# Performance work log

Hardware: AMD Instinct MI355X
Metric: run time of the kernel (lower is better)

Reference implementation:

```python
import jax, jax.numpy as jnp
import numpy as np


def setup_inputs() -> dict:
    key = jax.random.key(0)
    k0, k1, k2, k3 = jax.random.split(key, 4)
    B, T, D, F, E = 4, 2048, 512, 1024, 8
    x = jax.random.normal(k0, (B, T, D), dtype=jnp.float32)
    # router weight is zero-init in the original; use small random values so top-k
    router_w = 0.02 * jax.random.normal(k1, (E, D), dtype=jnp.float32)
    router_b = jnp.zeros((E,), dtype=jnp.float32)
    w_gate_up = 0.02 * jax.random.normal(k2, (E, D, 2 * F), dtype=jnp.float32)
    w_down = 0.02 * jax.random.normal(k3, (E, F, D), dtype=jnp.float32)
    return {"x": x, "router_w": router_w, "router_b": router_b,
            "w_gate_up": w_gate_up, "w_down": w_down, "top_k": 2}


def reference(x, router_w, router_b, w_gate_up, w_down, top_k):
    B, T, D = x.shape
    E = router_w.shape[0]
    x_flat = x.reshape(-1, D)                      # [N, D]
    N = x_flat.shape[0]

    # router: softmax over experts, top-k, renormalize
    logits = x_flat @ router_w.T + router_b       # [N, E]
    probs = jax.nn.softmax(logits, axis=-1)
    top_w, top_idx = jax.lax.top_k(probs, top_k)  # [N, k]
    top_w = top_w / jnp.sum(top_w, axis=-1, keepdims=True)

    # scatter renormalized weights into a dense [N, E] combine matrix
    combine = jnp.zeros((N, E), dtype=x.dtype).at[
        jnp.arange(N)[:, None], top_idx].add(top_w)

    # per-expert SwiGLU; combine weights zero out non-selected experts, giving
    # math identical to the sort/gather/scatter dispatch in the original
    out = jnp.zeros_like(x_flat)
    for e in range(E):  # fixed small expert count, not a data-dim loop
        gate_up = x_flat @ w_gate_up[e]           # [N, 2F]
        gate, up = jnp.split(gate_up, 2, axis=-1)
        h = jax.nn.silu(gate) * up                # [N, F]
        out = out + combine[:, e:e + 1] * (h @ w_down[e])
    return out.reshape(B, T, D)
```

## Files before the change

kernel.cpp:

```cpp
#include <hip/hip_runtime.h>
#include <stdint.h>

#define N_TOK 8192
#define D_DIM 512
#define F_DIM 1024
#define E_NUM 8
#define M_SLOTS (N_TOK * 2)

typedef __bf16 bf16x8 __attribute__((ext_vector_type(8)));
typedef float f32x4 __attribute__((ext_vector_type(4)));

__device__ __forceinline__ ushort f2b(float f) {
    union { float f; unsigned u; } v; v.f = f;
    unsigned r = v.u + 0x7fffu + ((v.u >> 16) & 1u);
    return (ushort)(r >> 16);
}
__device__ __forceinline__ float b2f(ushort u) {
    union { unsigned i; float f; } v; v.i = ((unsigned)u) << 16; return v.f;
}
__device__ __forceinline__ void gload16(const void* g, void* l) {
    __builtin_amdgcn_global_load_lds(
        (const __attribute__((address_space(1))) unsigned int*)g,
        (__attribute__((address_space(3))) unsigned int*)l, 16, 0, 0);
}

__global__ __launch_bounds__(256) void transpose_k(const float* __restrict__ in,
                                                   ushort* __restrict__ out,
                                                   int R, int C) {
    __shared__ ushort tile[64][65];
    int e = blockIdx.z;
    const float* src = in + (size_t)e * R * C;
    ushort* dst = out + (size_t)e * R * C;
    int c0 = blockIdx.x * 64, r0 = blockIdx.y * 64;
#pragma unroll
    for (int i = 0; i < 4; ++i) {
        int ch = threadIdx.x + i * 256;
        int row = ch >> 4, pos = ch & 15;
        float4 v = *(const float4*)(src + (size_t)(r0 + row) * C + c0 + pos * 4);
        tile[row][pos * 4 + 0] = f2b(v.x);
        tile[row][pos * 4 + 1] = f2b(v.y);
        tile[row][pos * 4 + 2] = f2b(v.z);
        tile[row][pos * 4 + 3] = f2b(v.w);
    }
    __syncthreads();
#pragma unroll
    for (int i = 0; i < 2; ++i) {
        int ch = threadIdx.x + i * 256;
        int ocol = ch >> 3, rb = ch & 7;
        ushort tmp[8];
#pragma unroll
        for (int j = 0; j < 8; ++j) tmp[j] = tile[rb * 8 + j][ocol];
        *(uint4*)(dst + (size_t)(c0 + ocol) * R + r0 + rb * 8) = *(const uint4*)tmp;
    }
}

__global__ __launch_bounds__(256) void logits_k(const float* __restrict__ x,
                                                const float* __restrict__ rw,
                                                const float* __restrict__ rb,
                                                ushort* __restrict__ x_bf,
                                                int* __restrict__ tok_e,
                                                float* __restrict__ tok_w,
                                                int* __restrict__ cnt) {
    if (blockIdx.x == 0 && threadIdx.x < 16) cnt[threadIdx.x] = 0;
    int lane = threadIdx.x & 63, wv = threadIdx.x >> 6;
    int t = blockIdx.x * 4 + wv;
    float4 xa = *(const float4*)(x + (size_t)t * D_DIM + lane * 8);
    float4 xb = *(const float4*)(x + (size_t)t * D_DIM + lane * 8 + 4);
    ushort u[8] = {f2b(xa.x), f2b(xa.y), f2b(xa.z), f2b(xa.w),
                   f2b(xb.x), f2b(xb.y), f2b(xb.z), f2b(xb.w)};
    *(uint4*)(x_bf + (size_t)t * D_DIM + lane * 8) = *(const uint4*)u;

    float acc[E_NUM];
#pragma unroll
    for (int e = 0; e < E_NUM; ++e) {
        float4 wa = *(const float4*)(rw + (size_t)e * D_DIM + lane * 8);
        float4 wb = *(const float4*)(rw + (size_t)e * D_DIM + lane * 8 + 4);
        float s = xa.x * wa.x + xa.y * wa.y + xa.z * wa.z + xa.w * wa.w +
                  xb.x * wb.x + xb.y * wb.y + xb.z * wb.z + xb.w * wb.w;
#pragma unroll
        for (int o = 32; o > 0; o >>= 1) s += __shfl_xor(s, o, 64);
        acc[e] = s;
    }
    if (lane == 0) {
        float l[E_NUM];
#pragma unroll
        for (int e = 0; e < E_NUM; ++e) l[e] = acc[e] + rb[e];
        int e0 = 0;
#pragma unroll
        for (int e = 1; e < E_NUM; ++e) if (l[e] > l[e0]) e0 = e;
        int e1 = (e0 == 0) ? 1 : 0;
#pragma unroll
        for (int e = 0; e < E_NUM; ++e) if (e != e0 && l[e] > l[e1]) e1 = e;
        float p1 = __expf(l[e1] - l[e0]);
        float w0 = 1.f / (1.f + p1), w1 = p1 / (1.f + p1);
        tok_e[2 * t] = e0;  tok_e[2 * t + 1] = e1;
        tok_w[2 * t] = w0;  tok_w[2 * t + 1] = w1;
    }
}

__global__ __launch_bounds__(256) void assign_k(const int* __restrict__ tok_e,
                                                int* __restrict__ cnt,
                                                int* __restrict__ rank) {
    __shared__ int lcnt[E_NUM], lbase[E_NUM];
    int tid = threadIdx.x;
    int i = blockIdx.x * 256 + tid;
    if (tid < E_NUM) lcnt[tid] = 0;
    __syncthreads();
    int e = tok_e[i];
    int intra = atomicAdd(&lcnt[e], 1);
    __syncthreads();
    if (tid < E_NUM) lbase[tid] = atomicAdd(&cnt[tid], lcnt[tid]);
    __syncthreads();
    rank[i] = lbase[e] + intra;
}

__global__ void prefix_k(const int* __restrict__ cnt, int* __restrict__ ebase) {
    if (threadIdx.x == 0) {
        int s = 0;
        for (int e = 0; e < E_NUM; ++e) { ebase[e] = s; s += cnt[e]; }
        ebase[E_NUM] = s;
    }
}

__global__ __launch_bounds__(256) void scatter_k(const int* __restrict__ tok_e,
                                                 const int* __restrict__ rank,
                                                 const int* __restrict__ ebase,
                                                 int* __restrict__ row_token,
                                                 int* __restrict__ tok_pos) {
    int i = blockIdx.x * 256 + threadIdx.x;
    int pos = ebase[tok_e[i]] + rank[i];
    row_token[pos] = i >> 1;
    tok_pos[i] = pos;
}

__global__ __launch_bounds__(256, 4) void gemm1_k(const ushort* __restrict__ x,
                                                  const ushort* __restrict__ wgu_t,
                                                  const int* __restrict__ ebase,
                                                  const int* __restrict__ row_token,
                                                  ushort* __restrict__ h) {
    int e = blockIdx.z;
    int base = ebase[e];
    int cnt = ebase[e + 1] - base;
    int tile0 = blockIdx.y * 128;
    if (tile0 >= cnt) return;
    int c0 = blockIdx.x * 64;

    __shared__ ushort smem[128 * 32 + 128 * 32];
    ushort* lds_a = smem;
    ushort* lds_b = smem + 128 * 32;

    int tid = threadIdx.x;
    int lane = tid & 63, wv = tid >> 6;
    int wr = wv >> 1, wc = wv & 1;

    const ushort* asrc[2];
    const ushort* bsrc[2];
#pragma unroll
    for (int i = 0; i < 2; ++i) {
        int c = tid + i * 256;
        int rp = c >> 3, s = c & 7;
        int lp = s ^ (rp & 7);
        int row = 2 * rp + (lp >> 2);
        int q = lp & 3;
        int r = tile0 + row;
        r = (r < cnt) ? r : (cnt - 1);
        int tok = row_token[base + r];
        asrc[i] = x + (size_t)tok * D_DIM + q * 8;
        int gc = (row < 64) ? (c0 + row) : (F_DIM + c0 + row - 64);
        bsrc[i] = wgu_t + ((size_t)e * (2 * F_DIM) + gc) * D_DIM + q * 8;
    }

    f32x4 accg[4][2], accu[4][2];
#pragma unroll
    for (int a = 0; a < 4; ++a)
#pragma unroll
        for (int b = 0; b < 2; ++b) {
            accg[a][b] = (f32x4){0.f, 0.f, 0.f, 0.f};
            accu[a][b] = (f32x4){0.f, 0.f, 0.f, 0.f};
        }

    int q = lane >> 4, m = lane & 15;
    int mh = m >> 1;
    int sl = (4 * (m & 1) + q) ^ (mh & 7);
    int soff = sl * 8;

    for (int k0 = 0; k0 < D_DIM; k0 += 32) {
        __syncthreads();
#pragma unroll
        for (int i = 0; i < 2; ++i) {
            int c = tid + i * 256;
            gload16(asrc[i] + k0, lds_a + (size_t)c * 8);
            gload16(bsrc[i] + k0, lds_b + (size_t)c * 8);
        }
        __syncthreads();

        bf16x8 af[4], bg[2], bu[2];
#pragma unroll
        for (int mt = 0; mt < 4; ++mt)
            af[mt] = *(const bf16x8*)(lds_a + (wr * 32 + mt * 8 + mh) * 64 + soff);
#pragma unroll
        for (int nt = 0; nt < 2; ++nt) {
            bg[nt] = *(const bf16x8*)(lds_b + (wc * 16 + nt * 8 + mh) * 64 + soff);
            bu[nt] = *(const bf16x8*)(lds_b + (32 + wc * 16 + nt * 8 + mh) * 64 + soff);
        }
#pragma unroll
        for (int mt = 0; mt < 4; ++mt)
#pragma unroll
            for (int nt = 0; nt < 2; ++nt) {
                accg[mt][nt] = __builtin_amdgcn_mfma_f32_16x16x32_bf16(af[mt], bg[nt], accg[mt][nt], 0, 0, 0);
                accu[mt][nt] = __builtin_amdgcn_mfma_f32_16x16x32_bf16(af[mt], bu[nt], accu[mt][nt], 0, 0, 0);
            }
    }

    ushort* stg = smem;
    int col = m;
    __syncthreads();
#pragma unroll
    for (int mt = 0; mt < 4; ++mt) {
#pragma unroll
        for (int nt = 0; nt < 2; ++nt) {
            int sc = wc * 32 + nt * 16 + col;
#pragma unroll
            for (int r4 = 0; r4 < 4; ++r4) {
                int sr = wr * 16 + q * 4 + r4;
                float g = accg[mt][nt][r4];
                float u = accu[mt][nt][r4];
                stg[sr * 68 + sc] = f2b((g / (1.f + __expf(-g))) * u);
            }
        }
        __syncthreads();
        {
            int sr = tid >> 3;
            int coff = (tid & 7) * 8;
            int grow = tile0 + (sr >> 4) * 64 + mt * 16 + (sr & 15);
            if (grow < cnt)
                *(uint4*)(h + (size_t)(base + grow) * F_DIM + c0 + coff) =
                    *(const uint4*)(stg + sr * 68 + coff);
        }
        __syncthreads();
    }
}

__global__ __launch_bounds__(256, 4) void gemm2_k(const ushort* __restrict__ h,
                                                  const ushort* __restrict__ wd_t,
                                                  const int* __restrict__ ebase,
                                                  ushort* __restrict__ slot) {
    int e = blockIdx.z;
    int base = ebase[e];
    int cnt = ebase[e + 1] - base;
    int tile0 = blockIdx.y * 128;
    if (tile0 >= cnt) return;
    int c0 = blockIdx.x * 128;

    __shared__ ushort smem[128 * 32 + 128 * 32];
    ushort* lds_a = smem;
    ushort* lds_b = smem + 128 * 32;

    int tid = threadIdx.x;
    int lane = tid & 63, wv = tid >> 6;
    int wr = wv >> 1, wc = wv & 1;

    const ushort* asrc[2]; const ushort* bsrc[2];
#pragma unroll
    for (int i = 0; i < 2; ++i) {
        int c = tid + i * 256;
        int rp = c >> 3, s = c & 7;
        int lp = s ^ (rp & 7);
        int row = 2 * rp + (lp >> 2);
        int q = lp & 3;
        int r = tile0 + row;
        r = (r < cnt) ? r : (cnt - 1);
        asrc[i] = h + (size_t)(base + r) * F_DIM + q * 8;
        bsrc[i] = wd_t + ((size_t)e * D_DIM + c0 + row) * F_DIM + q * 8;
    }

    f32x4 acc[4][4];
#pragma unroll
    for (int a = 0; a < 4; ++a)
#pragma unroll
        for (int b = 0; b < 4; ++b) acc[a][b] = (f32x4){0.f, 0.f, 0.f, 0.f};

    int q = lane >> 4, m = lane & 15;
    int mh = m >> 1;
    int sl = (4 * (m & 1) + q) ^ (mh & 7);
    int soff = sl * 8;

    for (int k0 = 0; k0 < F_DIM; k0 += 32) {
        __syncthreads();
#pragma unroll
        for (int i = 0; i < 2; ++i) {
            int c = tid + i * 256;
            gload16(asrc[i] + k0, lds_a + (size_t)c * 8);
            gload16(bsrc[i] + k0, lds_b + (size_t)c * 8);
        }
        __syncthreads();

        bf16x8 af[4], bb[4];
#pragma unroll
        for (int mt = 0; mt < 4; ++mt)
            af[mt] = *(const bf16x8*)(lds_a + (wr * 32 + mt * 8 + mh) * 64 + soff);
#pragma unroll
        for (int nt = 0; nt < 4; ++nt)
            bb[nt] = *(const bf16x8*)(lds_b + (wc * 32 + nt * 8 + mh) * 64 + soff);
#pragma unroll
        for (int mt = 0; mt < 4; ++mt)
#pragma unroll
            for (int nt = 0; nt < 4; ++nt)
                acc[mt][nt] = __builtin_amdgcn_mfma_f32_16x16x32_bf16(af[mt], bb[nt], acc[mt][nt], 0, 0, 0);
    }

    ushort* stg = smem;
    int col = m;
    __syncthreads();
#pragma unroll
    for (int mt = 0; mt < 4; ++mt) {
#pragma unroll
        for (int nt = 0; nt < 4; ++nt) {
            int scol = wc * 64 + nt * 16 + col;
#pragma unroll
            for (int r4 = 0; r4 < 4; ++r4) {
                int sr = wr * 16 + q * 4 + r4;
                stg[sr * 132 + scol] = f2b(acc[mt][nt][r4]);
            }
        }
        __syncthreads();
#pragma unroll
        for (int i = 0; i < 2; ++i) {
            int c = tid + i * 256;
            int sr = c >> 4;
            int coff = (c & 15) * 8;
            int grow = tile0 + (sr >> 4) * 64 + mt * 16 + (sr & 15);
            if (grow < cnt)
                *(uint4*)(slot + (size_t)(base + grow) * D_DIM + c0 + coff) =
                    *(const uint4*)(stg + sr * 132 + coff);
        }
        __syncthreads();
    }
}

__global__ __launch_bounds__(256) void combine_k(const ushort* __restrict__ slot,
                                                 const int* __restrict__ tok_pos,
                                                 const float* __restrict__ tok_w,
                                                 float* __restrict__ out) {
    int lane = threadIdx.x & 63, wv = threadIdx.x >> 6;
    int t = blockIdx.x * 4 + wv;
    int p0 = tok_pos[2 * t], p1 = tok_pos[2 * t + 1];
    float w0 = tok_w[2 * t], w1 = tok_w[2 * t + 1];
    uint4 s0 = *(const uint4*)(slot + (size_t)p0 * D_DIM + lane * 8);
    uint4 s1 = *(const uint4*)(slot + (size_t)p1 * D_DIM + lane * 8);
    const ushort* a = (const ushort*)&s0;
    const ushort* b = (const ushort*)&s1;
    float o[8];
#pragma unroll
    for (int j = 0; j < 8; ++j) o[j] = w0 * b2f(a[j]) + w1 * b2f(b[j]);
    float* dst = out + (size_t)t * D_DIM + lane * 8;
    *(float4*)dst = (float4){o[0], o[1], o[2], o[3]};
    *(float4*)(dst + 4) = (float4){o[4], o[5], o[6], o[7]};
}

extern "C" void kernel_launch(void* const* d_in, const int* in_sizes, int n_in,
                              void* d_out, int out_size, void* d_ws, size_t ws_size,
                              hipStream_t stream) {
    const float* x   = (const float*)d_in[0];
    const float* rw  = (const float*)d_in[1];
    const float* rb  = (const float*)d_in[2];
    const float* wgu = (const float*)d_in[3];
    const float* wd  = (const float*)d_in[4];
    float* out = (float*)d_out;

    char* ws = (char*)d_ws;
    size_t off = 0;
    auto alloc = [&](size_t bytes) -> void* {
        void* p = ws + off;
        off += (bytes + 255) & ~(size_t)255;
        return p;
    };
    ushort* wgu_t     = (ushort*)alloc((size_t)E_NUM * 2 * F_DIM * D_DIM * 2);
    ushort* wd_t      = (ushort*)alloc((size_t)E_NUM * D_DIM * F_DIM * 2);
    ushort* x_bf      = (ushort*)alloc((size_t)N_TOK * D_DIM * 2);
    ushort* hbuf      = (ushort*)alloc((size_t)M_SLOTS * F_DIM * 2);
    ushort* slot      = (ushort*)alloc((size_t)M_SLOTS * D_DIM * 2);
    int*    row_token = (int*)alloc(M_SLOTS * 4);
    int*    tok_e     = (int*)alloc(M_SLOTS * 4);
    int*    rankbuf   = (int*)alloc(M_SLOTS * 4);
    float*  tok_w     = (float*)alloc(M_SLOTS * 4);
    int*    tok_pos   = (int*)alloc(M_SLOTS * 4);
    int*    cnt       = (int*)alloc(64);
    int*    ebase     = (int*)alloc(64);

    logits_k<<<N_TOK / 4, 256, 0, stream>>>(x, rw, rb, x_bf, tok_e, tok_w, cnt);
    transpose_k<<<dim3(2 * F_DIM / 64, D_DIM / 64, E_NUM), 256, 0, stream>>>(wgu, wgu_t, D_DIM, 2 * F_DIM);
    transpose_k<<<dim3(D_DIM / 64, F_DIM / 64, E_NUM), 256, 0, stream>>>(wd, wd_t, F_DIM, D_DIM);
    assign_k<<<M_SLOTS / 256, 256, 0, stream>>>(tok_e, cnt, rankbuf);
    prefix_k<<<1, 64, 0, stream>>>(cnt, ebase);
    scatter_k<<<M_SLOTS / 256, 256, 0, stream>>>(tok_e, rankbuf, ebase, row_token, tok_pos);
    gemm1_k<<<dim3(16, 32, E_NUM), 256, 0, stream>>>(x_bf, wgu_t, ebase, row_token, hbuf);
    gemm2_k<<<dim3(4, 32, E_NUM), 256, 0, stream>>>(hbuf, wd_t, ebase, slot);
    combine_k<<<N_TOK / 4, 256, 0, stream>>>(slot, tok_pos, tok_w, out);
}
```

Measured before the change: 228.5 us.

## Triple-buffer MoE GEMM K-loops, fuse routing and weight-transpose launches

```diff
diff --git a/kernel.cpp b/kernel.cpp
--- a/kernel.cpp
+++ b/kernel.cpp
@@ -24,14 +24,25 @@
         (__attribute__((address_space(3))) unsigned int*)l, 16, 0, 0);
 }
 
-__global__ __launch_bounds__(256) void transpose_k(const float* __restrict__ in,
-                                                   ushort* __restrict__ out,
-                                                   int R, int C) {
+__global__ __launch_bounds__(256) void transpose_all_k(const float* __restrict__ wgu,
+                                                       ushort* __restrict__ wgu_t,
+                                                       const float* __restrict__ wd,
+                                                       ushort* __restrict__ wd_t) {
     __shared__ ushort tile[64][65];
-    int e = blockIdx.z;
-    const float* src = in + (size_t)e * R * C;
-    ushort* dst = out + (size_t)e * R * C;
-    int c0 = blockIdx.x * 64, r0 = blockIdx.y * 64;
+    int b = blockIdx.x;
+    const float* src; ushort* dst; int R, C, c0, r0;
+    if (b < 2048) {
+        int e = b >> 8, rem = b & 255;
+        R = D_DIM; C = 2 * F_DIM;
+        src = wgu + (size_t)e * R * C; dst = wgu_t + (size_t)e * R * C;
+        c0 = (rem & 31) * 64; r0 = (rem >> 5) * 64;
+    } else {
+        int b2 = b - 2048;
+        int e = b2 >> 7, rem = b2 & 127;
+        R = F_DIM; C = D_DIM;
+        src = wd + (size_t)e * R * C; dst = wd_t + (size_t)e * R * C;
+        c0 = (rem & 7) * 64; r0 = (rem >> 3) * 64;
+    }
 #pragma unroll
     for (int i = 0; i < 4; ++i) {
         int ch = threadIdx.x + i * 256;
@@ -59,9 +70,7 @@
                                                 const float* __restrict__ rb,
                                                 ushort* __restrict__ x_bf,
                                                 int* __restrict__ tok_e,
-                                                float* __restrict__ tok_w,
-                                                int* __restrict__ cnt) {
-    if (blockIdx.x == 0 && threadIdx.x < 16) cnt[threadIdx.x] = 0;
+                                                float* __restrict__ tok_w) {
     int lane = threadIdx.x & 63, wv = threadIdx.x >> 6;
     int t = blockIdx.x * 4 + wv;
     float4 xa = *(const float4*)(x + (size_t)t * D_DIM + lane * 8);
@@ -98,42 +107,50 @@
     }
 }
 
-__global__ __launch_bounds__(256) void assign_k(const int* __restrict__ tok_e,
-                                                int* __restrict__ cnt,
-                                                int* __restrict__ rank) {
-    __shared__ int lcnt[E_NUM], lbase[E_NUM];
-    int tid = threadIdx.x;
-    int i = blockIdx.x * 256 + tid;
+__global__ __launch_bounds__(1024) void route_k(const int* __restrict__ tok_e,
+                                                int* __restrict__ ebase,
+                                                int* __restrict__ row_token,
+                                                int* __restrict__ tok_pos) {
+    __shared__ int lcnt[E_NUM];
+    __shared__ int base_s[E_NUM];
+    int tid = threadIdx.x, lane = tid & 63;
     if (tid < E_NUM) lcnt[tid] = 0;
     __syncthreads();
-    int e = tok_e[i];
-    int intra = atomicAdd(&lcnt[e], 1);
-    __syncthreads();
-    if (tid < E_NUM) lbase[tid] = atomicAdd(&cnt[tid], lcnt[tid]);
-    __syncthreads();
-    rank[i] = lbase[e] + intra;
-}
-
-__global__ void prefix_k(const int* __restrict__ cnt, int* __restrict__ ebase) {
-    if (threadIdx.x == 0) {
+    int ev[16], intra[16];
+#pragma unroll
+    for (int j = 0; j < 16; ++j) {
+        int i = tid + j * 1024;
+        int e = tok_e[i];
+        unsigned long long m = ~0ull;
+#pragma unroll
+        for (int b = 0; b < 3; ++b) {
+            unsigned long long vb = __ballot(((e >> b) & 1) != 0);
+            m &= ((e >> b) & 1) ? vb : ~vb;
+        }
+        int prefix = __popcll(m & ((1ull << lane) - 1ull));
+        int leader = __ffsll((unsigned long long)m) - 1;
+        int bs = 0;
+        if (lane == leader) bs = atomicAdd(&lcnt[e], __popcll(m));
+        bs = __shfl(bs, leader, 64);
+        ev[j] = e; intra[j] = bs + prefix;
+    }
+    __syncthreads();
+    if (tid == 0) {
         int s = 0;
-        for (int e = 0; e < E_NUM; ++e) { ebase[e] = s; s += cnt[e]; }
+        for (int k = 0; k < E_NUM; ++k) { base_s[k] = s; ebase[k] = s; s += lcnt[k]; }
         ebase[E_NUM] = s;
     }
-}
-
-__global__ __launch_bounds__(256) void scatter_k(const int* __restrict__ tok_e,
-                                                 const int* __restrict__ rank,
-                                                 const int* __restrict__ ebase,
-                                                 int* __restrict__ row_token,
-                                                 int* __restrict__ tok_pos) {
-    int i = blockIdx.x * 256 + threadIdx.x;
-    int pos = ebase[tok_e[i]] + rank[i];
-    row_token[pos] = i >> 1;
-    tok_pos[i] = pos;
-}
-
-__global__ __launch_bounds__(256, 4) void gemm1_k(const ushort* __restrict__ x,
+    __syncthreads();
+#pragma unroll
+    for (int j = 0; j < 16; ++j) {
+        int i = tid + j * 1024;
+        int pos = base_s[ev[j]] + intra[j];
+        row_token[pos] = i >> 1;
+        tok_pos[i] = pos;
+    }
+}
+
+__global__ __launch_bounds__(256, 3) void gemm1_k(const ushort* __restrict__ x,
                                                   const ushort* __restrict__ wgu_t,
                                                   const int* __restrict__ ebase,
                                                   const int* __restrict__ row_token,
@@ -145,9 +162,7 @@
     if (tile0 >= cnt) return;
     int c0 = blockIdx.x * 64;
 
-    __shared__ ushort smem[128 * 32 + 128 * 32];
-    ushort* lds_a = smem;
-    ushort* lds_b = smem + 128 * 32;
+    __shared__ __align__(16) ushort smem[3 * 8192];
 
     int tid = threadIdx.x;
     int lane = tid & 63, wv = tid >> 6;
@@ -184,24 +199,24 @@
     int sl = (4 * (m & 1) + q) ^ (mh & 7);
     int soff = sl * 8;
 
-    for (int k0 = 0; k0 < D_DIM; k0 += 32) {
-        __syncthreads();
+    auto stage = [&](ushort* buf, int kk) {
 #pragma unroll
         for (int i = 0; i < 2; ++i) {
             int c = tid + i * 256;
-            gload16(asrc[i] + k0, lds_a + (size_t)c * 8);
-            gload16(bsrc[i] + k0, lds_b + (size_t)c * 8);
-        }
-        __syncthreads();
-
+            gload16(asrc[i] + kk, buf + (size_t)c * 8);
+            gload16(bsrc[i] + kk, buf + 4096 + (size_t)c * 8);
+        }
+    };
+    auto compute = [&](const ushort* la_) {
+        const ushort* lb_ = la_ + 4096;
         bf16x8 af[4], bg[2], bu[2];
 #pragma unroll
         for (int mt = 0; mt < 4; ++mt)
-            af[mt] = *(const bf16x8*)(lds_a + (wr * 32 + mt * 8 + mh) * 64 + soff);
+            af[mt] = *(const bf16x8*)(la_ + (wr * 32 + mt * 8 + mh) * 64 + soff);
 #pragma unroll
         for (int nt = 0; nt < 2; ++nt) {
-            bg[nt] = *(const bf16x8*)(lds_b + (wc * 16 + nt * 8 + mh) * 64 + soff);
-            bu[nt] = *(const bf16x8*)(lds_b + (32 + wc * 16 + nt * 8 + mh) * 64 + soff);
+            bg[nt] = *(const bf16x8*)(lb_ + (wc * 16 + nt * 8 + mh) * 64 + soff);
+            bu[nt] = *(const bf16x8*)(lb_ + (32 + wc * 16 + nt * 8 + mh) * 64 + soff);
         }
 #pragma unroll
         for (int mt = 0; mt < 4; ++mt)
@@ -210,38 +225,60 @@
                 accg[mt][nt] = __builtin_amdgcn_mfma_f32_16x16x32_bf16(af[mt], bg[nt], accg[mt][nt], 0, 0, 0);
                 accu[mt][nt] = __builtin_amdgcn_mfma_f32_16x16x32_bf16(af[mt], bu[nt], accu[mt][nt], 0, 0, 0);
             }
-    }
-
+    };
+
+    ushort* pc = smem;
+    ushort* pn = smem + 8192;
+    ushort* pf = smem + 16384;
+
+    stage(pc, 0);
+    stage(pn, 32);
+    asm volatile("s_waitcnt vmcnt(4) lgkmcnt(0)" ::: "memory");
+    __builtin_amdgcn_s_barrier();
+    __builtin_amdgcn_sched_barrier(0);
+
+    for (int k = 64; k <= D_DIM - 32; k += 32) {
+        stage(pf, k);
+        compute(pc);
+        asm volatile("s_waitcnt vmcnt(4) lgkmcnt(0)" ::: "memory");
+        __builtin_amdgcn_s_barrier();
+        __builtin_amdgcn_sched_barrier(0);
+        ushort* t_ = pc; pc = pn; pn = pf; pf = t_;
+    }
+    compute(pc);
+    asm volatile("s_waitcnt vmcnt(0) lgkmcnt(0)" ::: "memory");
+    __builtin_amdgcn_s_barrier();
+    __builtin_amdgcn_sched_barrier(0);
+    compute(pn);
+
+    __syncthreads();
     ushort* stg = smem;
-    int col = m;
-    __syncthreads();
-#pragma unroll
-    for (int mt = 0; mt < 4; ++mt) {
+#pragma unroll
+    for (int mt = 0; mt < 4; ++mt)
 #pragma unroll
         for (int nt = 0; nt < 2; ++nt) {
-            int sc = wc * 32 + nt * 16 + col;
+            int sc = wc * 32 + nt * 16 + m;
 #pragma unroll
             for (int r4 = 0; r4 < 4; ++r4) {
-                int sr = wr * 16 + q * 4 + r4;
+                int rr = wr * 64 + mt * 16 + q * 4 + r4;
                 float g = accg[mt][nt][r4];
                 float u = accu[mt][nt][r4];
-                stg[sr * 68 + sc] = f2b((g / (1.f + __expf(-g))) * u);
+                stg[rr * 68 + sc] = f2b((g / (1.f + __expf(-g))) * u);
             }
         }
-        __syncthreads();
-        {
-            int sr = tid >> 3;
-            int coff = (tid & 7) * 8;
-            int grow = tile0 + (sr >> 4) * 64 + mt * 16 + (sr & 15);
-            if (grow < cnt)
-                *(uint4*)(h + (size_t)(base + grow) * F_DIM + c0 + coff) =
-                    *(const uint4*)(stg + sr * 68 + coff);
-        }
-        __syncthreads();
-    }
-}
-
-__global__ __launch_bounds__(256, 4) void gemm2_k(const ushort* __restrict__ h,
+    __syncthreads();
+#pragma unroll
+    for (int p = 0; p < 4; ++p) {
+        int c = tid + p * 256;
+        int sr = c >> 3, coff = (c & 7) * 8;
+        int grow = tile0 + sr;
+        if (grow < cnt)
+            *(uint4*)(h + (size_t)(base + grow) * F_DIM + c0 + coff) =
+                *(const uint4*)(stg + sr * 68 + coff);
+    }
+}
+
+__global__ __launch_bounds__(256, 3) void gemm2_k(const ushort* __restrict__ h,
                                                   const ushort* __restrict__ wd_t,
                                                   const int* __restrict__ ebase,
                                                   ushort* __restrict__ slot) {
@@ -252,9 +289,7 @@
     if (tile0 >= cnt) return;
     int c0 = blockIdx.x * 128;
 
-    __shared__ ushort smem[128 * 32 + 128 * 32];
-    ushort* lds_a = smem;
-    ushort* lds_b = smem + 128 * 32;
+    __shared__ __align__(16) ushort smem[3 * 8192];
 
     int tid = threadIdx.x;
     int lane = tid & 63, wv = tid >> 6;
@@ -285,56 +320,76 @@
     int sl = (4 * (m & 1) + q) ^ (mh & 7);
     int soff = sl * 8;
 
-    for (int k0 = 0; k0 < F_DIM; k0 += 32) {
-        __syncthreads();
+    auto stage = [&](ushort* buf, int kk) {
 #pragma unroll
         for (int i = 0; i < 2; ++i) {
             int c = tid + i * 256;
-            gload16(asrc[i] + k0, lds_a + (size_t)c * 8);
-            gload16(bsrc[i] + k0, lds_b + (size_t)c * 8);
-        }
-        __syncthreads();
-
+            gload16(asrc[i] + kk, buf + (size_t)c * 8);
+            gload16(bsrc[i] + kk, buf + 4096 + (size_t)c * 8);
+        }
+    };
+    auto compute = [&](const ushort* la_) {
+        const ushort* lb_ = la_ + 4096;
         bf16x8 af[4], bb[4];
 #pragma unroll
         for (int mt = 0; mt < 4; ++mt)
-            af[mt] = *(const bf16x8*)(lds_a + (wr * 32 + mt * 8 + mh) * 64 + soff);
+            af[mt] = *(const bf16x8*)(la_ + (wr * 32 + mt * 8 + mh) * 64 + soff);
 #pragma unroll
         for (int nt = 0; nt < 4; ++nt)
-            bb[nt] = *(const bf16x8*)(lds_b + (wc * 32 + nt * 8 + mh) * 64 + soff);
+            bb[nt] = *(const bf16x8*)(lb_ + (wc * 32 + nt * 8 + mh) * 64 + soff);
 #pragma unroll
         for (int mt = 0; mt < 4; ++mt)
 #pragma unroll
             for (int nt = 0; nt < 4; ++nt)
                 acc[mt][nt] = __builtin_amdgcn_mfma_f32_16x16x32_bf16(af[mt], bb[nt], acc[mt][nt], 0, 0, 0);
-    }
-
+    };
+
+    ushort* pc = smem;
+    ushort* pn = smem + 8192;
+    ushort* pf = smem + 16384;
+
+    stage(pc, 0);
+    stage(pn, 32);
+    asm volatile("s_waitcnt vmcnt(4) lgkmcnt(0)" ::: "memory");
+    __builtin_amdgcn_s_barrier();
+    __builtin_amdgcn_sched_barrier(0);
+
+    for (int k = 64; k <= F_DIM - 32; k += 32) {
+        stage(pf, k);
+        compute(pc);
+        asm volatile("s_waitcnt vmcnt(4) lgkmcnt(0)" ::: "memory");
+        __builtin_amdgcn_s_barrier();
+        __builtin_amdgcn_sched_barrier(0);
+        ushort* t_ = pc; pc = pn; pn = pf; pf = t_;
+    }
+    compute(pc);
+    asm volatile("s_waitcnt vmcnt(0) lgkmcnt(0)" ::: "memory");
+    __builtin_amdgcn_s_barrier();
+    __builtin_amdgcn_sched_barrier(0);
+    compute(pn);
+
+    __syncthreads();
     ushort* stg = smem;
-    int col = m;
-    __syncthreads();
-#pragma unroll
-    for (int mt = 0; mt < 4; ++mt) {
+#pragma unroll
+    for (int mt = 0; mt < 4; ++mt)
 #pragma unroll
         for (int nt = 0; nt < 4; ++nt) {
-            int scol = wc * 64 + nt * 16 + col;
+            int scol = wc * 64 + nt * 16 + m;
 #pragma unroll
             for (int r4 = 0; r4 < 4; ++r4) {
-                int sr = wr * 16 + q * 4 + r4;
-                stg[sr * 132 + scol] = f2b(acc[mt][nt][r4]);
+                int rr = wr * 64 + mt * 16 + q * 4 + r4;
+                stg[rr * 132 + scol] = f2b(acc[mt][nt][r4]);
             }
         }
-        __syncthreads();
-#pragma unroll
-        for (int i = 0; i < 2; ++i) {
-            int c = tid + i * 256;
-            int sr = c >> 4;
-            int coff = (c & 15) * 8;
-            int grow = tile0 + (sr >> 4) * 64 + mt * 16 + (sr & 15);
-            if (grow < cnt)
-                *(uint4*)(slot + (size_t)(base + grow) * D_DIM + c0 + coff) =
-                    *(const uint4*)(stg + sr * 132 + coff);
-        }
-        __syncthreads();
+    __syncthreads();
+#pragma unroll
+    for (int p = 0; p < 8; ++p) {
+        int c = tid + p * 256;
+        int sr = c >> 4, coff = (c & 15) * 8;
+        int grow = tile0 + sr;
+        if (grow < cnt)
+            *(uint4*)(slot + (size_t)(base + grow) * D_DIM + c0 + coff) =
+                *(const uint4*)(stg + sr * 132 + coff);
     }
 }
 
@@ -382,18 +437,13 @@
     ushort* slot      = (ushort*)alloc((size_t)M_SLOTS * D_DIM * 2);
     int*    row_token = (int*)alloc(M_SLOTS * 4);
     int*    tok_e     = (int*)alloc(M_SLOTS * 4);
-    int*    rankbuf   = (int*)alloc(M_SLOTS * 4);
     float*  tok_w     = (float*)alloc(M_SLOTS * 4);
     int*    tok_pos   = (int*)alloc(M_SLOTS * 4);
-    int*    cnt       = (int*)alloc(64);
     int*    ebase     = (int*)alloc(64);
 
-    logits_k<<<N_TOK / 4, 256, 0, stream>>>(x, rw, rb, x_bf, tok_e, tok_w, cnt);
-    transpose_k<<<dim3(2 * F_DIM / 64, D_DIM / 64, E_NUM), 256, 0, stream>>>(wgu, wgu_t, D_DIM, 2 * F_DIM);
-    transpose_k<<<dim3(D_DIM / 64, F_DIM / 64, E_NUM), 256, 0, stream>>>(wd, wd_t, F_DIM, D_DIM);
-    assign_k<<<M_SLOTS / 256, 256, 0, stream>>>(tok_e, cnt, rankbuf);
-    prefix_k<<<1, 64, 0, stream>>>(cnt, ebase);
-    scatter_k<<<M_SLOTS / 256, 256, 0, stream>>>(tok_e, rankbuf, ebase, row_token, tok_pos);
+    logits_k<<<N_TOK / 4, 256, 0, stream>>>(x, rw, rb, x_bf, tok_e, tok_w);
+    transpose_all_k<<<3072, 256, 0, stream>>>(wgu, wgu_t, wd, wd_t);
+    route_k<<<1, 1024, 0, stream>>>(tok_e, ebase, row_token, tok_pos);
     gemm1_k<<<dim3(16, 32, E_NUM), 256, 0, stream>>>(x_bf, wgu_t, ebase, row_token, hbuf);
     gemm2_k<<<dim3(4, 32, E_NUM), 256, 0, stream>>>(hbuf, wd_t, ebase, slot);
     combine_k<<<N_TOK / 4, 256, 0, stream>>>(slot, tok_pos, tok_w, out);
```

Result: faster. 216.6 us (-5.2%).
